# Optimization experiments

Measured on AMD Instinct MI355X. Metric: run time of the kernel, lower is better.

The kernel has to match this reference:

```python
import jax, jax.numpy as jnp
import numpy as np

S = 8192          # number of segments (slices)
D = 64            # hidden_dimension
H = 1             # num_heads (must be 1 or D for the broadcast attn*x)


def _make_slices():
    # ragged but deterministic: alternate 64 / 192 -> total = S*128 = 1,048,576
    lens = np.where(np.arange(S) % 2 == 0, 64, 192).astype(np.int64)
    return lens


def setup_inputs() -> dict:
    key = jax.random.key(0)
    k1, k2, k3 = jax.random.split(key, 3)
    lens = _make_slices()
    b = int(lens.sum())  # 1048576
    x = jax.random.normal(k1, (b, D), dtype=jnp.float32)
    W = jax.random.normal(k2, (H, D + 1), dtype=jnp.float32) * 0.1
    bias = jax.random.normal(k3, (H,), dtype=jnp.float32) * 0.1
    return {"x": x, "slices": jnp.asarray(lens), "W": W, "bias": bias}


def reference(x, slices, W, bias):
    b, d = x.shape
    S_ = slices.shape[0]
    # segment ids for every row (b is static at trace time)
    seg_ids = jnp.repeat(jnp.arange(S_), slices, total_repeat_length=b)
    offsets = jnp.concatenate([jnp.zeros((1,), slices.dtype), jnp.cumsum(slices)[:-1]])
    # per-segment positional encoding: arange(n)/n
    pos = (jnp.arange(b) - offsets[seg_ids]).astype(x.dtype) / slices[seg_ids].astype(x.dtype)
    Phi = jnp.concatenate([pos[:, None], x], axis=1)          # [b, d+1]
    logits = Phi @ W.T + bias                                  # [b, H]
    # numerically stable segment softmax over each slice
    seg_max = jax.ops.segment_max(logits, seg_ids, num_segments=S_)
    e = jnp.exp(logits - seg_max[seg_ids])
    denom = jax.ops.segment_sum(e, seg_ids, num_segments=S_)
    attn = e / denom[seg_ids]                                  # [b, H]
    ctx = attn * x                                             # [b, d] (H==1 broadcast)
    pooled = jax.ops.segment_sum(ctx, seg_ids, num_segments=S_)  # [S, d]
    return pooled
```

## Files before the change

kernel.cpp:

```cpp
#include <hip/hip_runtime.h>
#include <math.h>

#define BLOCK 256
#define CHUNK_SHIFT 8
#define CHUNK (1 << CHUNK_SHIFT)

__global__ __launch_bounds__(BLOCK) void chunk_sum_kernel(const int* __restrict__ slices,
                                                          int S, int* __restrict__ chunkSums) {
    const int tid = threadIdx.x;
    const int idx = (blockIdx.x << CHUNK_SHIFT) + tid;
    int v = (idx < S) ? slices[idx] : 0;
#pragma unroll
    for (int m = 1; m < 64; m <<= 1) v += __shfl_xor(v, m, 64);
    __shared__ int ws[BLOCK / 64];
    if ((tid & 63) == 0) ws[tid >> 6] = v;
    __syncthreads();
    if (tid == 0) chunkSums[blockIdx.x] = ws[0] + ws[1] + ws[2] + ws[3];
}

__global__ __launch_bounds__(BLOCK, 8) void attn_pool_kernel(
    const float* __restrict__ x, const int* __restrict__ slices,
    const float* __restrict__ W, const float* __restrict__ bias,
    const int* __restrict__ chunkSums, float* __restrict__ out, int S) {
    __shared__ float4 combA[2][2][2][16];
    __shared__ float  combD[2][2][2];

    const int tid  = threadIdx.x;
    const int lane = tid & 63;
    const int wave = tid >> 6;
    const int pi   = wave >> 1;
    const int w    = wave & 1;
    const int pairId = (blockIdx.x << 1) + pi;
    const int s0   = pairId << 1;

    const int grp = lane >> 4;
    const int c0  = (lane & 15) << 2;
    const float w0 = W[1 + c0 + 0];
    const float w1 = W[1 + c0 + 1];
    const float w2 = W[1 + c0 + 2];
    const float w3 = W[1 + c0 + 3];
    const float Wpos = W[0];

    float4 acc0 = make_float4(0.f, 0.f, 0.f, 0.f);
    float4 acc1 = make_float4(0.f, 0.f, 0.f, 0.f);
    float den0 = 0.f, den1 = 0.f;

    if (s0 < S) {
        const int chunk = s0 >> CHUNK_SHIFT;
        int part = (lane < chunk) ? chunkSums[lane] : 0;
        const int cnt = s0 - (chunk << CHUNK_SHIFT);
        const int j   = (chunk << CHUNK_SHIFT) + (lane << 2);
        const int loc = lane << 2;
        if (j + 3 < S) {
            const int4 sv = *(const int4*)(slices + j);
            part += ((loc     < cnt) ? sv.x : 0)
                  + ((loc + 1 < cnt) ? sv.y : 0)
                  + ((loc + 2 < cnt) ? sv.z : 0)
                  + ((loc + 3 < cnt) ? sv.w : 0);
        } else {
#pragma unroll
            for (int e = 0; e < 4; ++e) {
                const int idx = j + e;
                if (idx < S && loc + e < cnt) part += slices[idx];
            }
        }
#pragma unroll
        for (int m = 1; m < 64; m <<= 1) part += __shfl_xor(part, m, 64);
        const size_t off = (size_t)part;

        const int n0 = slices[s0];
        const int n1 = (s0 + 1 < S) ? slices[s0 + 1] : 0;

        const int K0 = (n0 + 3) >> 2;
        const int K1 = (n1 + 3) >> 2;
        const int T  = K0 + K1;
        const int half = (T + 1) >> 1;
        const int t0 = w * half;
        const int t1 = min(T, t0 + half);

        const float pscale0 = Wpos / (float)n0;
        const float pscale1 = (n1 > 0) ? Wpos / (float)n1 : 0.f;

        const float4* __restrict__ base0 = (const float4*)x + off * 16 + lane;
        const float4* __restrict__ base1 = base0 + (size_t)n0 * 16;

        const int a = min(t1, K0);
#pragma unroll 4
        for (int t = t0; t < a; ++t) {
            const int r = (t << 2) + grp;
            if (r < n0) {
                const float4 v = base0[(size_t)t << 6];
                float p = fmaf(v.x, w0, fmaf(v.y, w1, fmaf(v.z, w2, v.w * w3)));
                p += __shfl_xor(p, 1, 64);
                p += __shfl_xor(p, 2, 64);
                p += __shfl_xor(p, 4, 64);
                p += __shfl_xor(p, 8, 64);
                const float e = __expf(fmaf((float)r, pscale0, p));
                acc0.x = fmaf(e, v.x, acc0.x);
                acc0.y = fmaf(e, v.y, acc0.y);
                acc0.z = fmaf(e, v.z, acc0.z);
                acc0.w = fmaf(e, v.w, acc0.w);
                den0 += e;
            }
        }
        const int b = max(t0, K0);
#pragma unroll 4
        for (int t = b; t < t1; ++t) {
            const int k = t - K0;
            const int r = (k << 2) + grp;
            if (r < n1) {
                const float4 v = base1[(size_t)k << 6];
                float p = fmaf(v.x, w0, fmaf(v.y, w1, fmaf(v.z, w2, v.w * w3)));
                p += __shfl_xor(p, 1, 64);
                p += __shfl_xor(p, 2, 64);
                p += __shfl_xor(p, 4, 64);
                p += __shfl_xor(p, 8, 64);
                const float e = __expf(fmaf((float)r, pscale1, p));
                acc1.x = fmaf(e, v.x, acc1.x);
                acc1.y = fmaf(e, v.y, acc1.y);
                acc1.z = fmaf(e, v.z, acc1.z);
                acc1.w = fmaf(e, v.w, acc1.w);
                den1 += e;
            }
        }
    }

#pragma unroll
    for (int m = 16; m < 64; m <<= 1) {
        acc0.x += __shfl_xor(acc0.x, m, 64);
        acc0.y += __shfl_xor(acc0.y, m, 64);
        acc0.z += __shfl_xor(acc0.z, m, 64);
        acc0.w += __shfl_xor(acc0.w, m, 64);
        acc1.x += __shfl_xor(acc1.x, m, 64);
        acc1.y += __shfl_xor(acc1.y, m, 64);
        acc1.z += __shfl_xor(acc1.z, m, 64);
        acc1.w += __shfl_xor(acc1.w, m, 64);
        den0   += __shfl_xor(den0,   m, 64);
        den1   += __shfl_xor(den1,   m, 64);
    }

    if (lane < 16) {
        combA[pi][w][0][lane] = acc0;
        combA[pi][w][1][lane] = acc1;
    }
    if (lane == 0) {
        combD[pi][w][0] = den0;
        combD[pi][w][1] = den1;
    }
    __syncthreads();

    const int po  = wave >> 1;
    const int seg = wave & 1;
    const int sOut = (((blockIdx.x << 1) + po) << 1) + seg;
    if (sOut < S && lane < 16) {
        const float4 a0 = combA[po][0][seg][lane];
        const float4 a1 = combA[po][1][seg][lane];
        const float inv = 1.f / (combD[po][0][seg] + combD[po][1][seg]);
        float4 r4;
        r4.x = (a0.x + a1.x) * inv;
        r4.y = (a0.y + a1.y) * inv;
        r4.z = (a0.z + a1.z) * inv;
        r4.w = (a0.w + a1.w) * inv;
        ((float4*)out)[(size_t)sOut * 16 + lane] = r4;
    }
}

extern "C" void kernel_launch(void* const* d_in, const int* in_sizes, int n_in,
                              void* d_out, int out_size, void* d_ws, size_t ws_size,
                              hipStream_t stream) {
    const float* x      = (const float*)d_in[0];
    const int*   slices = (const int*)d_in[1];
    const float* W      = (const float*)d_in[2];
    const float* bias   = (const float*)d_in[3];
    float*       out    = (float*)d_out;
    const int S = in_sizes[1];

    int* chunkSums = (int*)d_ws;

    const int nchunks = (S + CHUNK - 1) >> CHUNK_SHIFT;
    chunk_sum_kernel<<<nchunks, BLOCK, 0, stream>>>(slices, S, chunkSums);

    const int npairs = (S + 1) >> 1;
    const int grid   = (npairs + 1) >> 1;
    attn_pool_kernel<<<grid, BLOCK, 0, stream>>>(x, slices, W, bias, chunkSums, out, S);
}
```

Measured before the change: 51.83 us.

## Fuse prefix-sum into pooling kernel by per-block recomputation of segment offset

Removes the separate chunk-sum kernel launch and instead has each block compute its starting row offset by summing all preceding slice lengths with a block-wide int4 reduction. This eliminates a launch and the dependency between two kernels. In exchange each block redundantly reads up to S/4 int4 values (quadratic total work over blocks, mostly from L2), and a __syncthreads is added before the main loop. The int4 reads also assume s0 is a multiple of 4, which holds for this grid mapping.

```diff
diff --git a/kernel.cpp b/kernel.cpp
--- a/kernel.cpp
+++ b/kernel.cpp
@@ -2,36 +2,45 @@
 #include <math.h>
 
 #define BLOCK 256
-#define CHUNK_SHIFT 8
-#define CHUNK (1 << CHUNK_SHIFT)
 
-__global__ __launch_bounds__(BLOCK) void chunk_sum_kernel(const int* __restrict__ slices,
-                                                          int S, int* __restrict__ chunkSums) {
-    const int tid = threadIdx.x;
-    const int idx = (blockIdx.x << CHUNK_SHIFT) + tid;
-    int v = (idx < S) ? slices[idx] : 0;
-#pragma unroll
-    for (int m = 1; m < 64; m <<= 1) v += __shfl_xor(v, m, 64);
-    __shared__ int ws[BLOCK / 64];
-    if ((tid & 63) == 0) ws[tid >> 6] = v;
-    __syncthreads();
-    if (tid == 0) chunkSums[blockIdx.x] = ws[0] + ws[1] + ws[2] + ws[3];
-}
-
-__global__ __launch_bounds__(BLOCK, 8) void attn_pool_kernel(
+__global__ __launch_bounds__(BLOCK, 8) void attn_pool_fused(
     const float* __restrict__ x, const int* __restrict__ slices,
     const float* __restrict__ W, const float* __restrict__ bias,
-    const int* __restrict__ chunkSums, float* __restrict__ out, int S) {
+    float* __restrict__ out, int S) {
+    __shared__ int    wred[4];
     __shared__ float4 combA[2][2][2][16];
     __shared__ float  combD[2][2][2];
 
     const int tid  = threadIdx.x;
     const int lane = tid & 63;
     const int wave = tid >> 6;
-    const int pi   = wave >> 1;
-    const int w    = wave & 1;
-    const int pairId = (blockIdx.x << 1) + pi;
-    const int s0   = pairId << 1;
+    const int s0   = blockIdx.x << 2;
+
+    int part = 0;
+    {
+        const int cnt4 = s0 >> 2;
+        const int4* __restrict__ sl4 = (const int4*)slices;
+        for (int i = tid; i < cnt4; i += BLOCK) {
+            const int4 v = sl4[i];
+            part += v.x + v.y + v.z + v.w;
+        }
+#pragma unroll
+        for (int m = 1; m < 64; m <<= 1) part += __shfl_xor(part, m, 64);
+        if (lane == 0) wred[wave] = part;
+    }
+    __syncthreads();
+    const size_t P = (size_t)(wred[0] + wred[1] + wred[2] + wred[3]);
+
+    const int n0 = (s0     < S) ? slices[s0]     : 0;
+    const int n1 = (s0 + 1 < S) ? slices[s0 + 1] : 0;
+    const int n2 = (s0 + 2 < S) ? slices[s0 + 2] : 0;
+    const int n3 = (s0 + 3 < S) ? slices[s0 + 3] : 0;
+
+    const int pi = wave >> 1;
+    const int w  = wave & 1;
+    const int nA = pi ? n2 : n0;
+    const int nB = pi ? n3 : n1;
+    const size_t offA = pi ? (P + (size_t)(n0 + n1)) : P;
 
     const int grp = lane >> 4;
     const int c0  = (lane & 15) << 2;
@@ -45,83 +54,56 @@
     float4 acc1 = make_float4(0.f, 0.f, 0.f, 0.f);
     float den0 = 0.f, den1 = 0.f;
 
-    if (s0 < S) {
-        const int chunk = s0 >> CHUNK_SHIFT;
-        int part = (lane < chunk) ? chunkSums[lane] : 0;
-        const int cnt = s0 - (chunk << CHUNK_SHIFT);
-        const int j   = (chunk << CHUNK_SHIFT) + (lane << 2);
-        const int loc = lane << 2;
-        if (j + 3 < S) {
-            const int4 sv = *(const int4*)(slices + j);
-            part += ((loc     < cnt) ? sv.x : 0)
-                  + ((loc + 1 < cnt) ? sv.y : 0)
-                  + ((loc + 2 < cnt) ? sv.z : 0)
-                  + ((loc + 3 < cnt) ? sv.w : 0);
-        } else {
-#pragma unroll
-            for (int e = 0; e < 4; ++e) {
-                const int idx = j + e;
-                if (idx < S && loc + e < cnt) part += slices[idx];
-            }
+    const int K0 = (nA + 3) >> 2;
+    const int K1 = (nB + 3) >> 2;
+    const int T  = K0 + K1;
+    const int half = (T + 1) >> 1;
+    const int t0 = w * half;
+    const int t1 = min(T, t0 + half);
+
+    const float psA = nA ? (Wpos / (float)nA) : 0.f;
+    const float psB = nB ? (Wpos / (float)nB) : 0.f;
+
+    const float4* __restrict__ baseA = (const float4*)x + offA * 16 + lane;
+    const float4* __restrict__ baseB = baseA + (size_t)nA * 16;
+
+    const int ea = min(t1, K0);
+#pragma unroll 4
+    for (int t = t0; t < ea; ++t) {
+        const int r = (t << 2) + grp;
+        if (r < nA) {
+            const float4 v = baseA[(size_t)t << 6];
+            float p = fmaf(v.x, w0, fmaf(v.y, w1, fmaf(v.z, w2, v.w * w3)));
+            p += __shfl_xor(p, 1, 64);
+            p += __shfl_xor(p, 2, 64);
+            p += __shfl_xor(p, 4, 64);
+            p += __shfl_xor(p, 8, 64);
+            const float e = __expf(fmaf((float)r, psA, p));
+            acc0.x = fmaf(e, v.x, acc0.x);
+            acc0.y = fmaf(e, v.y, acc0.y);
+            acc0.z = fmaf(e, v.z, acc0.z);
+            acc0.w = fmaf(e, v.w, acc0.w);
+            den0 += e;
         }
-#pragma unroll
-        for (int m = 1; m < 64; m <<= 1) part += __shfl_xor(part, m, 64);
-        const size_t off = (size_t)part;
-
-        const int n0 = slices[s0];
-        const int n1 = (s0 + 1 < S) ? slices[s0 + 1] : 0;
-
-        const int K0 = (n0 + 3) >> 2;
-        const int K1 = (n1 + 3) >> 2;
-        const int T  = K0 + K1;
-        const int half = (T + 1) >> 1;
-        const int t0 = w * half;
-        const int t1 = min(T, t0 + half);
-
-        const float pscale0 = Wpos / (float)n0;
-        const float pscale1 = (n1 > 0) ? Wpos / (float)n1 : 0.f;
-
-        const float4* __restrict__ base0 = (const float4*)x + off * 16 + lane;
-        const float4* __restrict__ base1 = base0 + (size_t)n0 * 16;
-
-        const int a = min(t1, K0);
+    }
+    const int bb = max(t0, K0);
 #pragma unroll 4
-        for (int t = t0; t < a; ++t) {
-            const int r = (t << 2) + grp;
-            if (r < n0) {
-                const float4 v = base0[(size_t)t << 6];
-                float p = fmaf(v.x, w0, fmaf(v.y, w1, fmaf(v.z, w2, v.w * w3)));
-                p += __shfl_xor(p, 1, 64);
-                p += __shfl_xor(p, 2, 64);
-                p += __shfl_xor(p, 4, 64);
-                p += __shfl_xor(p, 8, 64);
-                const float e = __expf(fmaf((float)r, pscale0, p));
-                acc0.x = fmaf(e, v.x, acc0.x);
-                acc0.y = fmaf(e, v.y, acc0.y);
-                acc0.z = fmaf(e, v.z, acc0.z);
-                acc0.w = fmaf(e, v.w, acc0.w);
-                den0 += e;
-            }
-        }
-        const int b = max(t0, K0);
-#pragma unroll 4
-        for (int t = b; t < t1; ++t) {
-            const int k = t - K0;
-            const int r = (k << 2) + grp;
-            if (r < n1) {
-                const float4 v = base1[(size_t)k << 6];
-                float p = fmaf(v.x, w0, fmaf(v.y, w1, fmaf(v.z, w2, v.w * w3)));
-                p += __shfl_xor(p, 1, 64);
-                p += __shfl_xor(p, 2, 64);
-                p += __shfl_xor(p, 4, 64);
-                p += __shfl_xor(p, 8, 64);
-                const float e = __expf(fmaf((float)r, pscale1, p));
-                acc1.x = fmaf(e, v.x, acc1.x);
-                acc1.y = fmaf(e, v.y, acc1.y);
-                acc1.z = fmaf(e, v.z, acc1.z);
-                acc1.w = fmaf(e, v.w, acc1.w);
-                den1 += e;
-            }
+    for (int t = bb; t < t1; ++t) {
+        const int k = t - K0;
+        const int r = (k << 2) + grp;
+        if (r < nB) {
+            const float4 v = baseB[(size_t)k << 6];
+            float p = fmaf(v.x, w0, fmaf(v.y, w1, fmaf(v.z, w2, v.w * w3)));
+            p += __shfl_xor(p, 1, 64);
+            p += __shfl_xor(p, 2, 64);
+            p += __shfl_xor(p, 4, 64);
+            p += __shfl_xor(p, 8, 64);
+            const float e = __expf(fmaf((float)r, psB, p));
+            acc1.x = fmaf(e, v.x, acc1.x);
+            acc1.y = fmaf(e, v.y, acc1.y);
+            acc1.z = fmaf(e, v.z, acc1.z);
+            acc1.w = fmaf(e, v.w, acc1.w);
+            den1 += e;
         }
     }
 
@@ -149,9 +131,9 @@
     }
     __syncthreads();
 
-    const int po  = wave >> 1;
-    const int seg = wave & 1;
-    const int sOut = (((blockIdx.x << 1) + po) << 1) + seg;
+    const int po   = wave >> 1;
+    const int seg  = wave & 1;
+    const int sOut = s0 + (po << 1) + seg;
     if (sOut < S && lane < 16) {
         const float4 a0 = combA[po][0][seg][lane];
         const float4 a1 = combA[po][1][seg][lane];
@@ -175,12 +157,6 @@
     float*       out    = (float*)d_out;
     const int S = in_sizes[1];
 
-    int* chunkSums = (int*)d_ws;
-
-    const int nchunks = (S + CHUNK - 1) >> CHUNK_SHIFT;
-    chunk_sum_kernel<<<nchunks, BLOCK, 0, stream>>>(slices, S, chunkSums);
-
-    const int npairs = (S + 1) >> 1;
-    const int grid   = (npairs + 1) >> 1;
-    attn_pool_kernel<<<grid, BLOCK, 0, stream>>>(x, slices, W, bias, chunkSums, out, S);
+    const int grid = (S + 3) >> 2;
+    attn_pool_fused<<<grid, BLOCK, 0, stream>>>(x, slices, W, bias, out, S);
 }
```

New measurement: 48.35 us. 6.7% less time.
